# Performance work log

Hardware: AMD Instinct MI355X
Metric: run time of the kernel (lower is better)

The kernel has to match this reference:

```python
import jax, jax.numpy as jnp
import numpy as np

B, S, D, H, WIN, MAXLEN = 2, 2048, 512, 8, 7, 2048
DK = D // H


def _make_pe(max_len, d_model):
    pos = np.arange(max_len, dtype=np.float32)[:, None]
    div = np.exp(np.arange(0, d_model, 2, dtype=np.float32) * (-np.log(10000.0) / d_model))
    pe = np.zeros((max_len, d_model), dtype=np.float32)
    pe[:, 0::2] = np.sin(pos * div)
    pe[:, 1::2] = np.cos(pos * div)
    return jnp.asarray(pe)


def setup_inputs() -> dict:
    key = jax.random.key(0)
    ks = jax.random.split(key, 8)
    xavier = np.sqrt(6.0 / (D + D))  # xavier_uniform for square Linear
    def lin_w(k):
        return jax.random.uniform(k, (D, D), jnp.float32, -xavier, xavier)
    return {
        "x": jax.random.normal(ks[0], (B, S, D), jnp.float32),
        "mask": jnp.ones((B, S), dtype=bool),
        "wq_w": lin_w(ks[1]), "wq_b": jnp.zeros((D,), jnp.float32),
        "wk_w": lin_w(ks[2]), "wk_b": jnp.zeros((D,), jnp.float32),
        "wv_w": lin_w(ks[3]), "wv_b": jnp.zeros((D,), jnp.float32),
        "wo_w": lin_w(ks[4]), "wo_b": jnp.zeros((D,), jnp.float32),
        "ln_g": jnp.ones((D,), jnp.float32),
        "ln_b": jnp.zeros((D,), jnp.float32),
        "pe": _make_pe(MAXLEN, D),
    }


def reference(x, mask, wq_w, wq_b, wk_w, wk_b, wv_w, wv_b, wo_w, wo_b, ln_g, ln_b, pe):
    b, s, d = x.shape
    h, dk = H, DK
    half = WIN // 2
    residual = x
    xp = x + pe[:s][None, :, :]  # positional encoding

    def proj(w, bias):
        y = xp @ w.T + bias  # torch Linear: x W^T + b
        return y.reshape(b, s, h, dk).transpose(0, 2, 1, 3)  # [b,h,s,dk]

    Q, K, V = proj(wq_w, wq_b), proj(wk_w, wk_b), proj(wv_w, wv_b)

    scores = jnp.einsum("bhqd,bhkd->bhqk", Q, K) / jnp.sqrt(jnp.float32(dk))

    idx = jnp.arange(s)
    local = jnp.abs(idx[:, None] - idx[None, :]) <= half  # banded window mask [s,s]
    scores = jnp.where(local[None, None], scores, jnp.float32(-1e9))

    attn_mask = mask[:, None, :, None] & mask[:, None, None, :]  # [b,1,s,s]
    scores = jnp.where(attn_mask, scores, jnp.float32(-1e9))

    attn = jax.nn.softmax(scores, axis=-1)  # dropout is identity in eval
    out = jnp.einsum("bhqk,bhkd->bhqd", attn, V)
    out = out.transpose(0, 2, 1, 3).reshape(b, s, d)
    out = out @ wo_w.T + wo_b

    y = residual + out
    mu = jnp.mean(y, axis=-1, keepdims=True)
    var = jnp.mean((y - mu) ** 2, axis=-1, keepdims=True)
    y = (y - mu) / jnp.sqrt(var + 1e-5) * ln_g + ln_b
    return (y, attn)
```

## Files before the change

### kernel.cpp

```cpp
#include <hip/hip_runtime.h>
#include <math.h>

#define Bb 2
#define Ss 2048
#define Dd 512
#define Hh 8
#define DKk 64
#define HALF 3
#define MROWS (Bb*Ss)
#define KDIM 512

typedef __attribute__((ext_vector_type(8))) short short8;
typedef __attribute__((ext_vector_type(4))) float f32x4;

static __device__ inline unsigned short f2bf(float f) {
    union { float f; unsigned int u; } v; v.f = f;
    unsigned int r = v.u + 0x7FFFu + ((v.u >> 16) & 1u);
    return (unsigned short)(r >> 16);
}
static __device__ inline float bf2f(unsigned short h) {
    union { unsigned int u; float f; } v; v.u = ((unsigned int)h) << 16;
    return v.f;
}

static __device__ inline void gload_lds16(const unsigned short* gp, unsigned short* lp) {
    __builtin_amdgcn_global_load_lds(
        (const __attribute__((address_space(1))) unsigned int*)(gp),
        (__attribute__((address_space(3))) unsigned int*)(lp), 16, 0, 0);
}

#define WQ4 (512*512/4)
#define XP4 (MROWS*Dd/4)
__global__ __launch_bounds__(256) void prep_kernel(
    const float* __restrict__ wq, const float* __restrict__ wk,
    const float* __restrict__ wv, const float* __restrict__ wo,
    const float* __restrict__ bq, const float* __restrict__ bk,
    const float* __restrict__ bv,
    const float* __restrict__ x,  const float* __restrict__ pe,
    unsigned short* __restrict__ wqkv, unsigned short* __restrict__ wob,
    float* __restrict__ bqkv, unsigned short* __restrict__ xpb)
{
    const int i = blockIdx.x * 256 + threadIdx.x;
    if (i < 4 * WQ4) {
        const float* src = (i < WQ4) ? wq : (i < 2 * WQ4 ? wk : (i < 3 * WQ4 ? wv : wo));
        unsigned short* dst = (i < 3 * WQ4) ? wqkv : wob;
        int wi = (i < 3 * WQ4) ? i : (i - 3 * WQ4);
        float4 v = ((const float4*)src)[i % WQ4];
        ushort4 o = { f2bf(v.x), f2bf(v.y), f2bf(v.z), f2bf(v.w) };
        *(ushort4*)&dst[(size_t)wi * 4] = o;
    } else if (i < 4 * WQ4 + XP4) {
        int xi = i - 4 * WQ4;
        float4 a = ((const float4*)x)[xi];
        float4 p = ((const float4*)pe)[xi % (Ss * Dd / 4)];
        ushort4 o = { f2bf(a.x + p.x), f2bf(a.y + p.y), f2bf(a.z + p.z), f2bf(a.w + p.w) };
        *(ushort4*)&xpb[(size_t)xi * 4] = o;
    }
    if (i < 384) {
        const float* bsrc = (i < 128) ? bq : (i < 256 ? bk : bv);
        ((float4*)bqkv)[i] = ((const float4*)bsrc)[i & 127];
    }
}

#define BM 64
#define BN 128
#define BK 32

__global__ __launch_bounds__(256) void gemm_bf16_kernel(
    const unsigned short* __restrict__ A,
    const unsigned short* __restrict__ Bw,
    const float* __restrict__ bias,
    const float* __restrict__ resid,
    float* __restrict__ Cf,
    unsigned short* __restrict__ Cb,
    int ldc)
{
    __shared__ unsigned short As[BM * BK];
    __shared__ unsigned short Bs[BN * BK];
    const int tid = threadIdx.x;
    const int lane = tid & 63;
    const int wave = tid >> 6;
    const int wm = wave >> 1, wn = wave & 1;
    const int bm = blockIdx.y * BM;
    const int bn = blockIdx.x * BN;

    f32x4 acc[2][4] = {};

    const int srow = tid >> 2;
    const int scol = (tid & 3) * 8;
    const unsigned short* ga = A + (size_t)(bm + srow) * KDIM + scol;
    const unsigned short* gb = Bw + (size_t)(bn + srow) * KDIM + scol;

    for (int k0 = 0; k0 < KDIM; k0 += BK) {
        gload_lds16(ga + k0, &As[tid * 8]);
        gload_lds16(gb + k0, &Bs[tid * 8]);
        gload_lds16(gb + k0 + (size_t)64 * KDIM, &Bs[(tid + 256) * 8]);
        __syncthreads();

        const int lm = lane & 15;
        const int kq = lane >> 4;
        const unsigned short* pa = &As[(wm * 32 + lm) * BK + kq * 8];
        const unsigned short* pb = &Bs[(wn * 64 + lm) * BK + kq * 8];
        short8 af[2], bfr[4];
#pragma unroll
        for (int i = 0; i < 2; ++i) af[i] = *(const short8*)(pa + i * 16 * BK);
#pragma unroll
        for (int j = 0; j < 4; ++j) bfr[j] = *(const short8*)(pb + j * 16 * BK);
#pragma unroll
        for (int i = 0; i < 2; ++i)
#pragma unroll
            for (int j = 0; j < 4; ++j)
                acc[i][j] = __builtin_amdgcn_mfma_f32_16x16x32_bf16(af[i], bfr[j], acc[i][j], 0, 0, 0);
        __syncthreads();
    }

    const int lm = lane & 15;
    const int rq = lane >> 4;
#pragma unroll
    for (int i = 0; i < 2; ++i) {
#pragma unroll
        for (int j = 0; j < 4; ++j) {
            int col = bn + wn * 64 + j * 16 + lm;
            float bv = bias[col];
#pragma unroll
            for (int r = 0; r < 4; ++r) {
                int row = bm + wm * 32 + i * 16 + rq * 4 + r;
                float v = acc[i][j][r] + bv;
                if (resid) v += resid[(size_t)row * ldc + col];
                if (Cf) Cf[(size_t)row * ldc + col] = v;
                else    Cb[(size_t)row * ldc + col] = f2bf(v);
            }
        }
    }
}

__global__ __launch_bounds__(256) void attn_kernel(
    const unsigned short* __restrict__ QKV,
    float* __restrict__ attn_out,
    unsigned short* __restrict__ ctx)
{
    const int gid = blockIdx.x * 4 + (threadIdx.x >> 6);
    const int lane = threadIdx.x & 63;
    const int q = gid % Ss;
    const int h = (gid / Ss) % Hh;
    const int b = gid / (Ss * Hh);

    const size_t rowQ = (size_t)(b * Ss + q) * 1536 + h * DKk;
    const float qd = bf2f(QKV[rowQ + lane]);

    float sc[7];
    float m = -1e30f;
#pragma unroll
    for (int t = 0; t < 7; ++t) {
        int j = q - HALF + t;
        int jc = min(max(j, 0), Ss - 1);
        float kv = bf2f(QKV[(size_t)(b * Ss + jc) * 1536 + 512 + h * DKk + lane]);
        float prod = qd * kv;
#pragma unroll
        for (int off = 32; off; off >>= 1) prod += __shfl_xor(prod, off);
        sc[t] = (j >= 0 && j < Ss) ? prod * 0.125f : -1e30f;
        m = fmaxf(m, sc[t]);
    }
    float p[7];
    float denom = 0.f;
#pragma unroll
    for (int t = 0; t < 7; ++t) { p[t] = expf(sc[t] - m); denom += p[t]; }
    const float inv = 1.f / denom;
#pragma unroll
    for (int t = 0; t < 7; ++t) p[t] *= inv;

    float o = 0.f;
#pragma unroll
    for (int t = 0; t < 7; ++t) {
        int j = q - HALF + t;
        int jc = min(max(j, 0), Ss - 1);
        o += p[t] * bf2f(QKV[(size_t)(b * Ss + jc) * 1536 + 1024 + h * DKk + lane]);
    }
    ctx[(size_t)(b * Ss + q) * 512 + h * DKk + lane] = f2bf(o);

    const int lo = q - HALF;
    const int g0 = lo >> 2;
    const int r  = lo & 3;
    f32x4 Bv[3];
#pragma unroll
    for (int k = 0; k < 3; ++k) {
#pragma unroll
        for (int e = 0; e < 4; ++e) {
            int idx = k * 4 + e;
            int t = idx - r;
            int col = lo + t;
            float pv = 0.f;
            pv = (t == 0) ? p[0] : pv;
            pv = (t == 1) ? p[1] : pv;
            pv = (t == 2) ? p[2] : pv;
            pv = (t == 3) ? p[3] : pv;
            pv = (t == 4) ? p[4] : pv;
            pv = (t == 5) ? p[5] : pv;
            pv = (t == 6) ? p[6] : pv;
            Bv[k][e] = (t >= 0 && t < 7 && col >= 0 && col < Ss) ? pv : 0.f;
        }
    }
    const f32x4 zero4 = { 0.f, 0.f, 0.f, 0.f };
    f32x4* rowp = (f32x4*)(attn_out + ((((size_t)b * Hh + h) * Ss + q) * Ss));
#pragma unroll
    for (int v = 0; v < 8; ++v) {
        const int c4 = v * 64 + lane;
        const int sel = c4 - g0;
        f32x4 val = zero4;
        val = (sel == 0) ? Bv[0] : val;
        val = (sel == 1) ? Bv[1] : val;
        val = (sel == 2) ? Bv[2] : val;
        __builtin_nontemporal_store(val, rowp + c4);
    }
}

__global__ __launch_bounds__(256) void ln_kernel(const float* __restrict__ ypre,
                                                 const float* __restrict__ g,
                                                 const float* __restrict__ be,
                                                 float* __restrict__ yout) {
    __shared__ float sdata[8];
    const int row = blockIdx.x;
    const int tid = threadIdx.x;
    const float* r = ypre + (size_t)row * Dd;
    float v0 = r[tid], v1 = r[tid + 256];

    float s = v0 + v1;
#pragma unroll
    for (int off = 32; off; off >>= 1) s += __shfl_xor(s, off);
    if ((tid & 63) == 0) sdata[tid >> 6] = s;
    __syncthreads();
    float mu = (sdata[0] + sdata[1] + sdata[2] + sdata[3]) * (1.0f / Dd);
    __syncthreads();

    float d0 = v0 - mu, d1 = v1 - mu;
    float s2 = d0 * d0 + d1 * d1;
#pragma unroll
    for (int off = 32; off; off >>= 1) s2 += __shfl_xor(s2, off);
    if ((tid & 63) == 0) sdata[4 + (tid >> 6)] = s2;
    __syncthreads();
    float var = (sdata[4] + sdata[5] + sdata[6] + sdata[7]) * (1.0f / Dd);
    float rstd = rsqrtf(var + 1e-5f);

    yout[(size_t)row * Dd + tid]       = d0 * rstd * g[tid] + be[tid];
    yout[(size_t)row * Dd + tid + 256] = d1 * rstd * g[tid + 256] + be[tid + 256];
}

extern "C" void kernel_launch(void* const* d_in, const int* in_sizes, int n_in,
                              void* d_out, int out_size, void* d_ws, size_t ws_size,
                              hipStream_t stream) {
    const float* x  = (const float*)d_in[0];
    const float* wq = (const float*)d_in[2];
    const float* bq = (const float*)d_in[3];
    const float* wk = (const float*)d_in[4];
    const float* bk = (const float*)d_in[5];
    const float* wv = (const float*)d_in[6];
    const float* bv = (const float*)d_in[7];
    const float* wo = (const float*)d_in[8];
    const float* bo = (const float*)d_in[9];
    const float* g  = (const float*)d_in[10];
    const float* be = (const float*)d_in[11];
    const float* pe = (const float*)d_in[12];

    float* out_y    = (float*)d_out;
    float* out_attn = out_y + (size_t)Bb * Ss * Dd;

    char* w = (char*)d_ws;
    unsigned short* wqkv = (unsigned short*)(w);
    unsigned short* wob  = (unsigned short*)(w + 1572864);
    float*          bqkv = (float*)(w + 2097152);
    unsigned short* xpb  = (unsigned short*)(w + 2103296);
    unsigned short* QKVb = (unsigned short*)(w + 2103296 + 4194304);
    unsigned short* ctx  = (unsigned short*)(w + 2103296 + 4194304 + 12582912);
    float*          ypre = (float*)(w + 2103296 + 4194304 + 12582912 + 4194304);

    prep_kernel<<<(4 * WQ4 + XP4 + 255) / 256, 256, 0, stream>>>(
        wq, wk, wv, wo, bq, bk, bv, x, pe, wqkv, wob, bqkv, xpb);

    dim3 gqkv(1536 / BN, MROWS / BM);
    gemm_bf16_kernel<<<gqkv, 256, 0, stream>>>(xpb, wqkv, bqkv, nullptr, nullptr, QKVb, 1536);

    attn_kernel<<<(Bb * Hh * Ss) / 4, 256, 0, stream>>>(QKVb, out_attn, ctx);

    dim3 go(512 / BN, MROWS / BM);
    gemm_bf16_kernel<<<go, 256, 0, stream>>>(ctx, wob, bo, x, ypre, nullptr, 512);

    ln_kernel<<<MROWS, 256, 0, stream>>>(ypre, g, be, out_y);
}
```

Baseline: 346.1 us.

## Template GEMM tile height, pair queries per attention wave, store pre-LN output in bf16

The GEMM becomes a template over the M-tile height, and the QKV projection uses a 128-row tile to get more MFMA work per loaded B tile. The attention kernel now has each wave handle two adjacent queries, so 8 K/V rows are shared across both instead of loading 7 per query, and two attention-matrix rows are written per wave. The output projection writes its residual-added pre-LayerNorm result as bf16 rather than fp32, and the LN kernel reads bf16 pairs and writes float2. Rounding the residual sum to bf16 before LayerNorm adds precision error to the final output.

```diff
diff --git a/kernel.cpp b/kernel.cpp
--- a/kernel.cpp
+++ b/kernel.cpp
@@ -61,10 +61,10 @@
     }
 }
 
-#define BM 64
 #define BN 128
 #define BK 32
 
+template<int MI, bool OUT_BF16>
 __global__ __launch_bounds__(256) void gemm_bf16_kernel(
     const unsigned short* __restrict__ A,
     const unsigned short* __restrict__ Bw,
@@ -74,6 +74,7 @@
     unsigned short* __restrict__ Cb,
     int ldc)
 {
+    constexpr int BM = MI * 32;
     __shared__ unsigned short As[BM * BK];
     __shared__ unsigned short Bs[BN * BK];
     const int tid = threadIdx.x;
@@ -83,7 +84,7 @@
     const int bm = blockIdx.y * BM;
     const int bn = blockIdx.x * BN;
 
-    f32x4 acc[2][4] = {};
+    f32x4 acc[MI][4] = {};
 
     const int srow = tid >> 2;
     const int scol = (tid & 3) * 8;
@@ -92,21 +93,23 @@
 
     for (int k0 = 0; k0 < KDIM; k0 += BK) {
         gload_lds16(ga + k0, &As[tid * 8]);
+        if (MI == 4)
+            gload_lds16(ga + k0 + (size_t)64 * KDIM, &As[(tid + 256) * 8]);
         gload_lds16(gb + k0, &Bs[tid * 8]);
         gload_lds16(gb + k0 + (size_t)64 * KDIM, &Bs[(tid + 256) * 8]);
         __syncthreads();
 
         const int lm = lane & 15;
         const int kq = lane >> 4;
-        const unsigned short* pa = &As[(wm * 32 + lm) * BK + kq * 8];
+        const unsigned short* pa = &As[(wm * (MI * 16) + lm) * BK + kq * 8];
         const unsigned short* pb = &Bs[(wn * 64 + lm) * BK + kq * 8];
-        short8 af[2], bfr[4];
-#pragma unroll
-        for (int i = 0; i < 2; ++i) af[i] = *(const short8*)(pa + i * 16 * BK);
+        short8 af[MI], bfr[4];
+#pragma unroll
+        for (int i = 0; i < MI; ++i) af[i] = *(const short8*)(pa + i * 16 * BK);
 #pragma unroll
         for (int j = 0; j < 4; ++j) bfr[j] = *(const short8*)(pb + j * 16 * BK);
 #pragma unroll
-        for (int i = 0; i < 2; ++i)
+        for (int i = 0; i < MI; ++i)
 #pragma unroll
             for (int j = 0; j < 4; ++j)
                 acc[i][j] = __builtin_amdgcn_mfma_f32_16x16x32_bf16(af[i], bfr[j], acc[i][j], 0, 0, 0);
@@ -116,18 +119,18 @@
     const int lm = lane & 15;
     const int rq = lane >> 4;
 #pragma unroll
-    for (int i = 0; i < 2; ++i) {
+    for (int i = 0; i < MI; ++i) {
 #pragma unroll
         for (int j = 0; j < 4; ++j) {
             int col = bn + wn * 64 + j * 16 + lm;
             float bv = bias[col];
 #pragma unroll
             for (int r = 0; r < 4; ++r) {
-                int row = bm + wm * 32 + i * 16 + rq * 4 + r;
+                int row = bm + wm * (MI * 16) + i * 16 + rq * 4 + r;
                 float v = acc[i][j][r] + bv;
                 if (resid) v += resid[(size_t)row * ldc + col];
-                if (Cf) Cf[(size_t)row * ldc + col] = v;
-                else    Cb[(size_t)row * ldc + col] = f2bf(v);
+                if (OUT_BF16) Cb[(size_t)row * ldc + col] = f2bf(v);
+                else          Cf[(size_t)row * ldc + col] = v;
             }
         }
     }
@@ -138,90 +141,113 @@
     float* __restrict__ attn_out,
     unsigned short* __restrict__ ctx)
 {
-    const int gid = blockIdx.x * 4 + (threadIdx.x >> 6);
+    const int gidw = blockIdx.x * 4 + (threadIdx.x >> 6);
     const int lane = threadIdx.x & 63;
-    const int q = gid % Ss;
-    const int h = (gid / Ss) % Hh;
-    const int b = gid / (Ss * Hh);
-
-    const size_t rowQ = (size_t)(b * Ss + q) * 1536 + h * DKk;
-    const float qd = bf2f(QKV[rowQ + lane]);
-
-    float sc[7];
-    float m = -1e30f;
+    const int qp = gidw & 1023;
+    const int q0 = qp * 2;
+    const int h = (gidw >> 10) & 7;
+    const int b = gidw >> 13;
+
+    const int base = b * Ss;
+    const int hoff = h * DKk;
+    const float qd0 = bf2f(QKV[(size_t)(base + q0) * 1536 + hoff + lane]);
+    const float qd1 = bf2f(QKV[(size_t)(base + q0 + 1) * 1536 + hoff + lane]);
+
+    float s0[7], s1[7];
+    float m0 = -1e30f, m1 = -1e30f;
+#pragma unroll
+    for (int t = 0; t < 8; ++t) {
+        int j = q0 - HALF + t;
+        int jc = min(max(j, 0), Ss - 1);
+        float kv = bf2f(QKV[(size_t)(base + jc) * 1536 + 512 + hoff + lane]);
+        float pr0 = qd0 * kv, pr1 = qd1 * kv;
+#pragma unroll
+        for (int off = 32; off; off >>= 1) {
+            pr0 += __shfl_xor(pr0, off);
+            pr1 += __shfl_xor(pr1, off);
+        }
+        bool valid = (j >= 0) && (j < Ss);
+        if (t < 7) { s0[t] = valid ? pr0 * 0.125f : -1e30f; m0 = fmaxf(m0, s0[t]); }
+        if (t > 0) { s1[t - 1] = valid ? pr1 * 0.125f : -1e30f; m1 = fmaxf(m1, s1[t - 1]); }
+    }
+    float p0[7], p1[7];
+    float d0 = 0.f, d1 = 0.f;
 #pragma unroll
     for (int t = 0; t < 7; ++t) {
-        int j = q - HALF + t;
+        p0[t] = expf(s0[t] - m0); d0 += p0[t];
+        p1[t] = expf(s1[t] - m1); d1 += p1[t];
+    }
+    const float i0 = 1.f / d0, i1 = 1.f / d1;
+#pragma unroll
+    for (int t = 0; t < 7; ++t) { p0[t] *= i0; p1[t] *= i1; }
+
+    float o0 = 0.f, o1 = 0.f;
+#pragma unroll
+    for (int t = 0; t < 8; ++t) {
+        int j = q0 - HALF + t;
         int jc = min(max(j, 0), Ss - 1);
-        float kv = bf2f(QKV[(size_t)(b * Ss + jc) * 1536 + 512 + h * DKk + lane]);
-        float prod = qd * kv;
-#pragma unroll
-        for (int off = 32; off; off >>= 1) prod += __shfl_xor(prod, off);
-        sc[t] = (j >= 0 && j < Ss) ? prod * 0.125f : -1e30f;
-        m = fmaxf(m, sc[t]);
-    }
-    float p[7];
-    float denom = 0.f;
-#pragma unroll
-    for (int t = 0; t < 7; ++t) { p[t] = expf(sc[t] - m); denom += p[t]; }
-    const float inv = 1.f / denom;
-#pragma unroll
-    for (int t = 0; t < 7; ++t) p[t] *= inv;
-
-    float o = 0.f;
-#pragma unroll
-    for (int t = 0; t < 7; ++t) {
-        int j = q - HALF + t;
-        int jc = min(max(j, 0), Ss - 1);
-        o += p[t] * bf2f(QKV[(size_t)(b * Ss + jc) * 1536 + 1024 + h * DKk + lane]);
-    }
-    ctx[(size_t)(b * Ss + q) * 512 + h * DKk + lane] = f2bf(o);
-
-    const int lo = q - HALF;
-    const int g0 = lo >> 2;
-    const int r  = lo & 3;
-    f32x4 Bv[3];
+        float vv = bf2f(QKV[(size_t)(base + jc) * 1536 + 1024 + hoff + lane]);
+        if (t < 7) o0 += p0[t] * vv;
+        if (t > 0) o1 += p1[t - 1] * vv;
+    }
+    ctx[(size_t)(base + q0) * 512 + hoff + lane] = f2bf(o0);
+    ctx[(size_t)(base + q0 + 1) * 512 + hoff + lane] = f2bf(o1);
+
+    const int lo0 = q0 - HALF, lo1 = q0 + 1 - HALF;
+    const int g00 = lo0 >> 2, g01 = lo1 >> 2;
+    const int r0 = lo0 & 3,  r1 = lo1 & 3;
+    f32x4 Bv0[3], Bv1[3];
 #pragma unroll
     for (int k = 0; k < 3; ++k) {
 #pragma unroll
         for (int e = 0; e < 4; ++e) {
             int idx = k * 4 + e;
-            int t = idx - r;
-            int col = lo + t;
-            float pv = 0.f;
-            pv = (t == 0) ? p[0] : pv;
-            pv = (t == 1) ? p[1] : pv;
-            pv = (t == 2) ? p[2] : pv;
-            pv = (t == 3) ? p[3] : pv;
-            pv = (t == 4) ? p[4] : pv;
-            pv = (t == 5) ? p[5] : pv;
-            pv = (t == 6) ? p[6] : pv;
-            Bv[k][e] = (t >= 0 && t < 7 && col >= 0 && col < Ss) ? pv : 0.f;
+            {
+                int t = idx - r0; int col = lo0 + t;
+                float pv = 0.f;
+                pv = (t == 0) ? p0[0] : pv; pv = (t == 1) ? p0[1] : pv;
+                pv = (t == 2) ? p0[2] : pv; pv = (t == 3) ? p0[3] : pv;
+                pv = (t == 4) ? p0[4] : pv; pv = (t == 5) ? p0[5] : pv;
+                pv = (t == 6) ? p0[6] : pv;
+                Bv0[k][e] = (t >= 0 && t < 7 && col >= 0 && col < Ss) ? pv : 0.f;
+            }
+            {
+                int t = idx - r1; int col = lo1 + t;
+                float pv = 0.f;
+                pv = (t == 0) ? p1[0] : pv; pv = (t == 1) ? p1[1] : pv;
+                pv = (t == 2) ? p1[2] : pv; pv = (t == 3) ? p1[3] : pv;
+                pv = (t == 4) ? p1[4] : pv; pv = (t == 5) ? p1[5] : pv;
+                pv = (t == 6) ? p1[6] : pv;
+                Bv1[k][e] = (t >= 0 && t < 7 && col >= 0 && col < Ss) ? pv : 0.f;
+            }
         }
     }
     const f32x4 zero4 = { 0.f, 0.f, 0.f, 0.f };
-    f32x4* rowp = (f32x4*)(attn_out + ((((size_t)b * Hh + h) * Ss + q) * Ss));
+    f32x4* rowp0 = (f32x4*)(attn_out + ((((size_t)b * Hh + h) * Ss + q0) * Ss));
+    f32x4* rowp1 = rowp0 + (Ss / 4);
 #pragma unroll
     for (int v = 0; v < 8; ++v) {
         const int c4 = v * 64 + lane;
-        const int sel = c4 - g0;
-        f32x4 val = zero4;
-        val = (sel == 0) ? Bv[0] : val;
-        val = (sel == 1) ? Bv[1] : val;
-        val = (sel == 2) ? Bv[2] : val;
-        __builtin_nontemporal_store(val, rowp + c4);
-    }
-}
-
-__global__ __launch_bounds__(256) void ln_kernel(const float* __restrict__ ypre,
+        const int se0 = c4 - g00, se1 = c4 - g01;
+        f32x4 v0 = zero4, v1 = zero4;
+        v0 = (se0 == 0) ? Bv0[0] : v0; v0 = (se0 == 1) ? Bv0[1] : v0; v0 = (se0 == 2) ? Bv0[2] : v0;
+        v1 = (se1 == 0) ? Bv1[0] : v1; v1 = (se1 == 1) ? Bv1[1] : v1; v1 = (se1 == 2) ? Bv1[2] : v1;
+        __builtin_nontemporal_store(v0, rowp0 + c4);
+        __builtin_nontemporal_store(v1, rowp1 + c4);
+    }
+}
+
+__global__ __launch_bounds__(256) void ln_kernel(const unsigned short* __restrict__ ypre,
                                                  const float* __restrict__ g,
                                                  const float* __restrict__ be,
                                                  float* __restrict__ yout) {
     __shared__ float sdata[8];
     const int row = blockIdx.x;
     const int tid = threadIdx.x;
-    const float* r = ypre + (size_t)row * Dd;
-    float v0 = r[tid], v1 = r[tid + 256];
+    const unsigned short* r = ypre + (size_t)row * Dd;
+    unsigned int pair = *(const unsigned int*)&r[2 * tid];
+    float v0 = bf2f((unsigned short)(pair & 0xFFFFu));
+    float v1 = bf2f((unsigned short)(pair >> 16));
 
     float s = v0 + v1;
 #pragma unroll
@@ -240,8 +266,9 @@
     float var = (sdata[4] + sdata[5] + sdata[6] + sdata[7]) * (1.0f / Dd);
     float rstd = rsqrtf(var + 1e-5f);
 
-    yout[(size_t)row * Dd + tid]       = d0 * rstd * g[tid] + be[tid];
-    yout[(size_t)row * Dd + tid + 256] = d1 * rstd * g[tid + 256] + be[tid + 256];
+    float2 outv = { d0 * rstd * g[2 * tid] + be[2 * tid],
+                    d1 * rstd * g[2 * tid + 1] + be[2 * tid + 1] };
+    *(float2*)&yout[(size_t)row * Dd + 2 * tid] = outv;
 }
 
 extern "C" void kernel_launch(void* const* d_in, const int* in_sizes, int n_in,
@@ -270,18 +297,20 @@
     unsigned short* xpb  = (unsigned short*)(w + 2103296);
     unsigned short* QKVb = (unsigned short*)(w + 2103296 + 4194304);
     unsigned short* ctx  = (unsigned short*)(w + 2103296 + 4194304 + 12582912);
-    float*          ypre = (float*)(w + 2103296 + 4194304 + 12582912 + 4194304);
+    unsigned short* ypre = (unsigned short*)(w + 2103296 + 4194304 + 12582912 + 4194304);
 
     prep_kernel<<<(4 * WQ4 + XP4 + 255) / 256, 256, 0, stream>>>(
         wq, wk, wv, wo, bq, bk, bv, x, pe, wqkv, wob, bqkv, xpb);
 
-    dim3 gqkv(1536 / BN, MROWS / BM);
-    gemm_bf16_kernel<<<gqkv, 256, 0, stream>>>(xpb, wqkv, bqkv, nullptr, nullptr, QKVb, 1536);
-
-    attn_kernel<<<(Bb * Hh * Ss) / 4, 256, 0, stream>>>(QKVb, out_attn, ctx);
-
-    dim3 go(512 / BN, MROWS / BM);
-    gemm_bf16_kernel<<<go, 256, 0, stream>>>(ctx, wob, bo, x, ypre, nullptr, 512);
+    dim3 gqkv(1536 / BN, MROWS / 128);
+    gemm_bf16_kernel<4, true><<<gqkv, 256, 0, stream>>>(
+        xpb, wqkv, bqkv, nullptr, nullptr, QKVb, 1536);
+
+    attn_kernel<<<(Bb * Hh * Ss / 2) / 4, 256, 0, stream>>>(QKVb, out_attn, ctx);
+
+    dim3 go(512 / BN, MROWS / 64);
+    gemm_bf16_kernel<2, true><<<go, 256, 0, stream>>>(
+        ctx, wob, bo, x, nullptr, ypre, 512);
 
     ln_kernel<<<MROWS, 256, 0, stream>>>(ypre, g, be, out_y);
 }
```

After: 349.4 us. About the same (+1.0%).
